# Kernel optimization log

Measured on AMD Instinct MI355X. Metric: run time of the kernel, lower is better.

The kernel has to match this reference:

```python
import jax, jax.numpy as jnp
import numpy as np

N = 100000   # nodes
E = 1600000  # edges
F = 128      # input features
H = 128      # hidden
O = 64       # output classes
BN_EPS = 1e-5


def gcn_conv(x, edge_index, W, b, n_nodes):
    """PyG-style GCNConv: h = D^-1/2 (A+I) D^-1/2 (x W) + b."""
    h = x @ W  # [N, out]
    row = jnp.concatenate([edge_index[0], jnp.arange(n_nodes)])  # add self loops
    col = jnp.concatenate([edge_index[1], jnp.arange(n_nodes)])
    deg = jax.ops.segment_sum(jnp.ones_like(row, dtype=h.dtype), row, num_segments=n_nodes)
    dinv = jnp.where(deg > 0, jax.lax.rsqrt(deg), 0.0)
    norm = dinv[row] * dinv[col]                 # [E+N]
    msg = h[col] * norm[:, None]                 # gather + scale
    out = jax.ops.segment_sum(msg, row, num_segments=n_nodes)  # scatter-add
    return out + b


def batch_norm(x, gamma, beta):
    mean = jnp.mean(x, axis=0)
    var = jnp.var(x, axis=0)
    return (x - mean) * jax.lax.rsqrt(var + BN_EPS) * gamma + beta


def setup_inputs() -> dict:
    key = jax.random.key(0)
    ks = jax.random.split(key, 10)
    x = jax.random.normal(ks[0], (N, F), dtype=jnp.float32)
    edge_index = jax.random.randint(ks[1], (2, E), 0, N, dtype=jnp.int64)
    W1 = jax.random.normal(ks[2], (F, H), dtype=jnp.float32) / np.sqrt(F)
    b1 = jnp.zeros((H,), dtype=jnp.float32)
    gamma1 = jnp.ones((H,), dtype=jnp.float32)
    beta1 = jnp.zeros((H,), dtype=jnp.float32)
    W2 = jax.random.normal(ks[3], (H, H), dtype=jnp.float32) / np.sqrt(H)
    b2 = jnp.zeros((H,), dtype=jnp.float32)
    W3 = jax.random.normal(ks[4], (H, O), dtype=jnp.float32) / np.sqrt(H)
    b3 = jnp.zeros((O,), dtype=jnp.float32)
    return {"x": x, "edge_index": edge_index, "W1": W1, "b1": b1,
            "gamma1": gamma1, "beta1": beta1, "W2": W2, "b2": b2,
            "W3": W3, "b3": b3}


def reference(x, edge_index, W1, b1, gamma1, beta1, W2, b2, W3, b3):
    h = gcn_conv(x, edge_index, W1, b1, N)
    h = jax.nn.relu(batch_norm(h, gamma1, beta1))
    h = gcn_conv(h, edge_index, W2, b2, N)
    h = jax.nn.relu(h)
    out = h @ W3 + b3  # final Linear classifier head [N, O]
    return out
```

## Files before the change

kernel.cpp:

```cpp
#include <hip/hip_runtime.h>

#define NN 100000
#define EE 1600000
#define HN 128
#define OO 64
#define SB 256
#define NBUCK 196
#define CH 4096

typedef __attribute__((ext_vector_type(8))) short bf16x8;
typedef __attribute__((ext_vector_type(4))) float f32x4;

__device__ __forceinline__ unsigned short f2bf(float f){
  unsigned u = __float_as_uint(f);
  return (unsigned short)((u + 0x7FFFu + ((u >> 16) & 1u)) >> 16);
}
__device__ __forceinline__ float bflo(unsigned u){ return __uint_as_float(u << 16); }
__device__ __forceinline__ float bfhi(unsigned u){ return __uint_as_float(u & 0xFFFF0000u); }

__global__ __launch_bounds__(256) void k_histpack(const int* __restrict__ rows, int* __restrict__ bcnt,
                                                  const float* __restrict__ W1, const float* __restrict__ W2,
                                                  const float* __restrict__ W3,
                                                  unsigned short* __restrict__ Wp1, unsigned short* __restrict__ Wp2,
                                                  unsigned short* __restrict__ Wp3){
  __shared__ int h[NBUCK];
  for (int i = threadIdx.x; i < NBUCK; i += 256) h[i] = 0;
  __syncthreads();
  int base = blockIdx.x * CH;
  for (int j = threadIdx.x; j < CH; j += 256){
    int e = base + j;
    if (e < EE) atomicAdd(&h[rows[e] >> 9], 1);
  }
  __syncthreads();
  for (int i = threadIdx.x; i < NBUCK; i += 256){
    int v = h[i];
    if (v) atomicAdd(&bcnt[i], v);
  }
  int b = blockIdx.x;
  if (b < 20){
    const float* W; unsigned short* Wp; int outc, i0;
    if (b < 8)      { W=W1; Wp=Wp1; outc=128; i0 = b*256; }
    else if (b < 16){ W=W2; Wp=Wp2; outc=128; i0 = (b-8)*256; }
    else            { W=W3; Wp=Wp3; outc=64;  i0 = (b-16)*256; }
    int i = i0 + threadIdx.x;
    if (i < 16*outc){
      int kb = i / outc, n = i - kb*outc;
      unsigned pk[4];
      #pragma unroll
      for (int jj = 0; jj < 4; ++jj){
        unsigned lo = f2bf(W[(size_t)(kb*8 + 2*jj)*outc + n]);
        unsigned hi = f2bf(W[(size_t)(kb*8 + 2*jj+1)*outc + n]);
        pk[jj] = lo | (hi << 16);
      }
      *reinterpret_cast<uint4*>(Wp + (size_t)i*8) = make_uint4(pk[0],pk[1],pk[2],pk[3]);
    }
  }
}

__global__ __launch_bounds__(64) void k_bscan(const int* __restrict__ bcnt,
                                              int* __restrict__ bbase, int* __restrict__ bcur){
  int lane = threadIdx.x;
  int run = 0;
  for (int c = 0; c < NBUCK; c += 64){
    int i = c + lane;
    int v = (i < NBUCK) ? bcnt[i] : 0;
    int s = v;
    #pragma unroll
    for (int d = 1; d < 64; d <<= 1){ int u = __shfl_up(s, d); if (lane >= d) s += u; }
    if (i < NBUCK){ bbase[i] = run + s - v; bcur[i] = run + s - v; }
    run += __shfl(s, 63);
  }
}

__global__ __launch_bounds__(256) void k_bucket(const int* __restrict__ rows, const int* __restrict__ cols,
                                                int* __restrict__ bcur, uint2* __restrict__ ebuf){
  __shared__ int bc[NBUCK];
  __shared__ int boff[NBUCK];
  __shared__ int ccur[NBUCK];
  __shared__ int gbase[NBUCK];
  __shared__ uint2 stage[CH];
  const int t = threadIdx.x;
  const int base = blockIdx.x * CH;
  const int nval = min(CH, EE - base);

  for (int i = t; i < NBUCK; i += 256) bc[i] = 0;
  __syncthreads();

  int er[16], ec[16];
  #pragma unroll
  for (int j = 0; j < 16; ++j){
    int i = j*256 + t;
    if (i < nval){
      er[j] = rows[base+i]; ec[j] = cols[base+i];
      atomicAdd(&bc[er[j] >> 9], 1);
    } else er[j] = -1;
  }
  __syncthreads();

  if (t < 64){
    int lane = t, run = 0;
    for (int c = 0; c < NBUCK; c += 64){
      int i = c + lane;
      int v = (i < NBUCK) ? bc[i] : 0;
      int s = v;
      #pragma unroll
      for (int d = 1; d < 64; d <<= 1){ int u = __shfl_up(s, d); if (lane >= d) s += u; }
      if (i < NBUCK) boff[i] = run + s - v;
      run += __shfl(s, 63);
    }
  }
  __syncthreads();
  if (t < NBUCK){
    gbase[t] = bc[t] ? atomicAdd(&bcur[t], bc[t]) : 0;
    ccur[t]  = boff[t];
  }
  __syncthreads();
  #pragma unroll
  for (int j = 0; j < 16; ++j){
    if (er[j] >= 0){
      int b = er[j] >> 9;
      int p = atomicAdd(&ccur[b], 1);
      stage[p] = make_uint2((unsigned)er[j], (unsigned)ec[j]);
    }
  }
  __syncthreads();
  for (int i = t; i < nval; i += 256){
    uint2 e = stage[i];
    int b = (int)(e.x >> 9);
    ebuf[gbase[b] + (i - boff[b])] = e;
  }
}

__global__ __launch_bounds__(256) void k_build(const uint2* __restrict__ ebuf,
                                               const int* __restrict__ bbase, const int* __restrict__ bcnt,
                                               int* __restrict__ row_start, int* __restrict__ cnt,
                                               float* __restrict__ dinv, int* __restrict__ csr_col){
  __shared__ int hist[512];
  __shared__ int cur[512];
  const int b = blockIdx.x;
  const int row0 = b << 9;
  const int nrow = min(512, NN - row0);
  const int ebase = bbase[b];
  const int ne = bcnt[b];
  const int t = threadIdx.x;

  for (int i = t; i < nrow; i += 256) hist[i] = 0;
  __syncthreads();
  for (int i = t; i < ne; i += 256)
    atomicAdd(&hist[(int)ebuf[ebase+i].x - row0], 1);
  __syncthreads();

  if (t < 64){
    int lane = t, run = 0;
    for (int c = 0; c < nrow; c += 64){
      int i = c + lane;
      int v = (i < nrow) ? hist[i] : 0;
      int s = v;
      #pragma unroll
      for (int d = 1; d < 64; d <<= 1){ int u = __shfl_up(s, d); if (lane >= d) s += u; }
      if (i < nrow) cur[i] = run + s - v;
      run += __shfl(s, 63);
    }
  }
  __syncthreads();
  for (int i = t; i < nrow; i += 256){
    int h = hist[i];
    int r = row0 + i;
    cnt[r] = h;
    dinv[r] = rsqrtf((float)(h+1));
    row_start[r] = ebase + cur[i];
    cur[i] += ebase;
  }
  __syncthreads();
  for (int i = t; i < ne; i += 256){
    uint2 e = ebuf[ebase+i];
    int p = atomicAdd(&cur[(int)e.x - row0], 1);
    csr_col[p] = (int)e.y;
  }
}

template<bool BF16OUT>
__global__ __launch_bounds__(256) void k_agg(const unsigned* __restrict__ h,
                                             const int* __restrict__ row_start,
                                             const int* __restrict__ cnt,
                                             const int* __restrict__ col,
                                             const float* __restrict__ dinv,
                                             const float* __restrict__ bias,
                                             void* __restrict__ outv){
  int wib  = __builtin_amdgcn_readfirstlane((int)(threadIdx.x >> 6));
  int wid  = blockIdx.x*4 + wib;
  int lane = threadIdx.x & 63;
  if (wid >= NN) return;
  int s = row_start[wid];
  int e = s + cnt[wid];
  float dr = dinv[wid];
  const unsigned* hp = h + lane;
  float ax, ay;
  {
    unsigned u = hp[(size_t)wid*64];
    ax = bflo(u); ay = bfhi(u);
  }
  int p = s;
  for (; p+7 < e; p += 8){
    unsigned uu[8];
    #pragma unroll
    for (int j=0;j<8;++j) uu[j] = hp[(size_t)col[p+j]*64];
    #pragma unroll
    for (int j=0;j<8;++j){ ax += bflo(uu[j]); ay += bfhi(uu[j]); }
  }
  for (; p+3 < e; p += 4){
    unsigned uu[4];
    #pragma unroll
    for (int j=0;j<4;++j) uu[j] = hp[(size_t)col[p+j]*64];
    #pragma unroll
    for (int j=0;j<4;++j){ ax += bflo(uu[j]); ay += bfhi(uu[j]); }
  }
  for (; p < e; ++p){
    unsigned u = hp[(size_t)col[p]*64];
    ax += bflo(u); ay += bfhi(u);
  }
  float2 bb = *reinterpret_cast<const float2*>(bias + 2*lane);
  float ox = ax*dr + bb.x, oy = ay*dr + bb.y;
  if constexpr (BF16OUT){
    ((unsigned*)outv)[(size_t)wid*64 + lane] = (unsigned)f2bf(ox) | ((unsigned)f2bf(oy) << 16);
  } else {
    *reinterpret_cast<float2*>((float*)outv + (size_t)wid*HN + 2*lane) = make_float2(ox, oy);
  }
}

template<int OUTC, int XFORM, bool ADD_BIAS, bool BF16OUT, bool ABF16>
__global__ __launch_bounds__(256) void k_mgemm(const void* __restrict__ Av,
                                               const unsigned short* __restrict__ Wp,
                                               const float* __restrict__ scale,
                                               const float* __restrict__ shiftv,
                                               const float* __restrict__ bias,
                                               const float* __restrict__ dinv,
                                               void* __restrict__ Cv){
  __shared__ char AsB[32768];
  const int t = threadIdx.x;
  const int row0 = blockIdx.x * 128;

  if constexpr (ABF16){
    const uint4* A = (const uint4*)Av;
    const int c8 = t & 15;
    const int k0 = c8*8;
    float sc[8], sh[8];
    if (XFORM == 1){
      #pragma unroll
      for (int j=0;j<8;++j){ sc[j]=scale[k0+j]; sh[j]=shiftv[k0+j]; }
    }
    #pragma unroll
    for (int g = 0; g < 8; ++g){
      int f = g*256 + t;
      int r = f >> 4;
      int row = row0 + r;
      int rc = row < NN ? row : NN-1;
      uint4 q = A[(size_t)rc*16 + c8];
      float vf[8] = { bflo(q.x),bfhi(q.x),bflo(q.y),bfhi(q.y),
                      bflo(q.z),bfhi(q.z),bflo(q.w),bfhi(q.w) };
      if (XFORM == 1){
        #pragma unroll
        for (int j=0;j<8;++j) vf[j] = fmaxf(fmaf(vf[j], sc[j], sh[j]), 0.f);
      } else if (XFORM == 2){
        #pragma unroll
        for (int j=0;j<8;++j) vf[j] = fmaxf(vf[j], 0.f);
      }
      unsigned pk[4];
      #pragma unroll
      for (int j=0;j<4;++j)
        pk[j] = (unsigned)f2bf(vf[2*j]) | ((unsigned)f2bf(vf[2*j+1]) << 16);
      int boff = (c8*16) ^ ((r & 7) << 4);
      *reinterpret_cast<uint4*>(AsB + r*256 + boff) = make_uint4(pk[0],pk[1],pk[2],pk[3]);
    }
  } else {
    const float* A = (const float*)Av;
    #pragma unroll
    for (int g = 0; g < 16; ++g){
      int f = g*256 + t;
      int r = f >> 5;
      int c4 = f & 31;
      int row = row0 + r;
      int rc = row < NN ? row : NN-1;
      float4 v = *reinterpret_cast<const float4*>(A + (size_t)rc*HN + c4*4);
      if (XFORM == 2){
        v.x = fmaxf(v.x, 0.f); v.y = fmaxf(v.y, 0.f);
        v.z = fmaxf(v.z, 0.f); v.w = fmaxf(v.w, 0.f);
      }
      unsigned p0 = (unsigned)f2bf(v.x) | ((unsigned)f2bf(v.y) << 16);
      unsigned p1 = (unsigned)f2bf(v.z) | ((unsigned)f2bf(v.w) << 16);
      int boff = (c4*8) ^ ((r & 7) << 4);
      *reinterpret_cast<uint2*>(AsB + r*256 + boff) = make_uint2(p0, p1);
    }
  }
  __syncthreads();

  const int wv = t >> 6;
  const int l  = t & 63;
  const int lm = l & 15;
  const int lk = l >> 4;
  constexpr int NF = OUTC/16;

  f32x4 acc[2][NF];
  #pragma unroll
  for (int mi=0;mi<2;++mi)
    #pragma unroll
    for (int ni=0;ni<NF;++ni) acc[mi][ni] = (f32x4){0.f,0.f,0.f,0.f};

  const bf16x8* WpV = reinterpret_cast<const bf16x8*>(Wp);

  #pragma unroll
  for (int ks = 0; ks < 4; ++ks){
    bf16x8 af[2];
    #pragma unroll
    for (int mi=0;mi<2;++mi){
      int R = wv*32 + mi*16 + lm;
      int boff = (ks*64 + lk*16) ^ ((R & 7) << 4);
      af[mi] = *reinterpret_cast<const bf16x8*>(AsB + R*256 + boff);
    }
    int kb = ks*4 + lk;
    #pragma unroll
    for (int ni=0;ni<NF;++ni){
      int n = ni*16 + lm;
      bf16x8 bfr = WpV[kb*OUTC + n];
      acc[0][ni] = __builtin_amdgcn_mfma_f32_16x16x32_bf16(af[0], bfr, acc[0][ni], 0,0,0);
      acc[1][ni] = __builtin_amdgcn_mfma_f32_16x16x32_bf16(af[1], bfr, acc[1][ni], 0,0,0);
    }
  }

  #pragma unroll
  for (int mi=0;mi<2;++mi){
    #pragma unroll
    for (int j=0;j<4;++j){
      int grow = row0 + wv*32 + mi*16 + lk*4 + j;
      if (grow >= NN) continue;
      if constexpr (BF16OUT){
        float dr = dinv[grow];
        unsigned short* po = (unsigned short*)Cv + (size_t)grow*OUTC;
        #pragma unroll
        for (int ni=0;ni<NF;++ni)
          po[ni*16 + lm] = f2bf(acc[mi][ni][j] * dr);
      } else {
        float* po = (float*)Cv + (size_t)grow*OUTC;
        #pragma unroll
        for (int ni=0;ni<NF;++ni){
          float v = acc[mi][ni][j];
          if (ADD_BIAS) v += bias[ni*16 + lm];
          po[ni*16 + lm] = v;
        }
      }
    }
  }
}

__global__ __launch_bounds__(256) void k_stats(const unsigned* __restrict__ a,
                                               float* __restrict__ ps, float* __restrict__ pq){
  __shared__ float l0[256], l1[256], m0[256], m1[256];
  int c = threadIdx.x & 63;
  int grp = threadIdx.x >> 6;
  float s0=0.f,s1=0.f,q0=0.f,q1=0.f;
  for (int r = blockIdx.x*4 + grp; r < NN; r += SB*4){
    unsigned u = a[(size_t)r*64 + c];
    float v0 = bflo(u), v1 = bfhi(u);
    s0 += v0; s1 += v1; q0 = fmaf(v0,v0,q0); q1 = fmaf(v1,v1,q1);
  }
  l0[threadIdx.x]=s0; l1[threadIdx.x]=s1; m0[threadIdx.x]=q0; m1[threadIdx.x]=q1;
  __syncthreads();
  if (grp==0){
    #pragma unroll
    for (int g=1;g<4;++g){ s0+=l0[g*64+c]; s1+=l1[g*64+c]; q0+=m0[g*64+c]; q1+=m1[g*64+c]; }
    ps[blockIdx.x*128 + 2*c]   = s0; ps[blockIdx.x*128 + 2*c+1] = s1;
    pq[blockIdx.x*128 + 2*c]   = q0; pq[blockIdx.x*128 + 2*c+1] = q1;
  }
}

__global__ __launch_bounds__(128) void k_bnfinal(const float* __restrict__ ps, const float* __restrict__ pq,
                                                 const float* __restrict__ gamma, const float* __restrict__ beta,
                                                 float* __restrict__ scale, float* __restrict__ shiftv){
  int c = threadIdx.x;
  float s=0.f, q=0.f;
  for (int b=0;b<SB;b++){ s += ps[b*128+c]; q += pq[b*128+c]; }
  float mean = s * (1.0f/NN);
  float var  = q * (1.0f/NN) - mean*mean;
  float inv  = rsqrtf(var + 1e-5f);
  float sc = gamma[c]*inv;
  scale[c]  = sc;
  shiftv[c] = beta[c] - mean*sc;
}

extern "C" void kernel_launch(void* const* d_in, const int* in_sizes, int n_in,
                              void* d_out, int out_size, void* d_ws, size_t ws_size,
                              hipStream_t stream) {
  const float* x      = (const float*)d_in[0];
  const int*   ei     = (const int*)d_in[1];
  const int*   rows   = ei;
  const int*   cols   = ei + EE;
  const float* W1     = (const float*)d_in[2];
  const float* b1     = (const float*)d_in[3];
  const float* gamma1 = (const float*)d_in[4];
  const float* beta1  = (const float*)d_in[5];
  const float* W2     = (const float*)d_in[6];
  const float* b2     = (const float*)d_in[7];
  const float* W3     = (const float*)d_in[8];
  const float* b3     = (const float*)d_in[9];
  float* out = (float*)d_out;

  char* w = (char*)d_ws;
  float* buf0      = (float*)w; w += (size_t)NN*HN*4;
  float* buf1      = (float*)w; w += (size_t)NN*HN*4;
  int*   csr_col   = (int*)w;   w += (size_t)EE*4;
  int*   row_start = (int*)w;   w += (size_t)NN*4;
  int*   cnt       = (int*)w;   w += (size_t)NN*4;
  float* dinv      = (float*)w; w += (size_t)NN*4;
  float* ps        = (float*)w; w += (size_t)SB*128*4;
  float* pq        = (float*)w; w += (size_t)SB*128*4;
  float* scale     = (float*)w; w += 1024;
  float* shiftv    = (float*)w; w += 1024;
  int*   bcnt      = (int*)w;   w += 1024;
  int*   bbase     = (int*)w;   w += 1024;
  int*   bcur      = (int*)w;   w += 1024;
  unsigned short* Wp1 = (unsigned short*)w; w += 128*128*2;
  unsigned short* Wp2 = (unsigned short*)w; w += 128*128*2;
  unsigned short* Wp3 = (unsigned short*)w; w += 128*64*2;
  uint2*    ebuf  = (uint2*)buf0;
  unsigned* hbf   = (unsigned*)buf0;
  unsigned* abf   = (unsigned*)buf1;

  (void)hipMemsetAsync(bcnt, 0, NBUCK*4, stream);

  const int CB = (EE + CH - 1)/CH, GB = (NN+127)/128, AB = NN/4;

  k_histpack<<<CB, 256, 0, stream>>>(rows, bcnt, W1, W2, W3, Wp1, Wp2, Wp3);
  k_bscan <<<1, 64, 0, stream>>>(bcnt, bbase, bcur);
  k_bucket<<<CB, 256, 0, stream>>>(rows, cols, bcur, ebuf);
  k_build <<<NBUCK, 256, 0, stream>>>(ebuf, bbase, bcnt, row_start, cnt, dinv, csr_col);

  k_mgemm<128,0,false,true,false><<<GB, 256, 0, stream>>>(x, Wp1, nullptr, nullptr, nullptr, dinv, hbf);
  k_agg<true><<<AB, 256, 0, stream>>>(hbf, row_start, cnt, csr_col, dinv, b1, abf);
  k_stats<<<SB, 256, 0, stream>>>(abf, ps, pq);
  k_bnfinal<<<1, 128, 0, stream>>>(ps, pq, gamma1, beta1, scale, shiftv);

  k_mgemm<128,1,false,true,true><<<GB, 256, 0, stream>>>(abf, Wp2, scale, shiftv, nullptr, dinv, hbf);
  k_agg<true><<<AB, 256, 0, stream>>>(hbf, row_start, cnt, csr_col, dinv, b2, abf);

  k_mgemm<64,2,true,false,true><<<GB, 256, 0, stream>>>(abf, Wp3, nullptr, nullptr, b3, nullptr, out);
}
```

Measured before the change: 274.1 us.

## Bucket edges into fixed-size slabs to drop histogram and scan passes

Edge bucketing now writes into fixed per-bucket slabs (SLAB entries each) using per-bucket atomic cursors. This removes the separate histogram kernel and the global bucket scan, and k_build computes its CSR base by summing the counts of earlier buckets. Each edge is also packed into a single 32-bit word (local row in the upper bits, column in the low 17 bits), which halves the staging traffic. The risk is overflow if any bucket receives more than SLAB edges, which is safe only for the roughly uniform random graph used here. Template parameters were also simplified.

```diff
diff --git a/kernel.cpp b/kernel.cpp
--- a/kernel.cpp
+++ b/kernel.cpp
@@ -7,6 +7,7 @@
 #define SB 256
 #define NBUCK 196
 #define CH 4096
+#define SLAB 16384
 
 typedef __attribute__((ext_vector_type(8))) short bf16x8;
 typedef __attribute__((ext_vector_type(4))) float f32x4;
@@ -18,31 +19,76 @@
 __device__ __forceinline__ float bflo(unsigned u){ return __uint_as_float(u << 16); }
 __device__ __forceinline__ float bfhi(unsigned u){ return __uint_as_float(u & 0xFFFF0000u); }
 
-__global__ __launch_bounds__(256) void k_histpack(const int* __restrict__ rows, int* __restrict__ bcnt,
-                                                  const float* __restrict__ W1, const float* __restrict__ W2,
-                                                  const float* __restrict__ W3,
-                                                  unsigned short* __restrict__ Wp1, unsigned short* __restrict__ Wp2,
-                                                  unsigned short* __restrict__ Wp3){
-  __shared__ int h[NBUCK];
-  for (int i = threadIdx.x; i < NBUCK; i += 256) h[i] = 0;
-  __syncthreads();
-  int base = blockIdx.x * CH;
-  for (int j = threadIdx.x; j < CH; j += 256){
-    int e = base + j;
-    if (e < EE) atomicAdd(&h[rows[e] >> 9], 1);
-  }
-  __syncthreads();
-  for (int i = threadIdx.x; i < NBUCK; i += 256){
-    int v = h[i];
-    if (v) atomicAdd(&bcnt[i], v);
-  }
+__global__ __launch_bounds__(256) void k_bucket(const int* __restrict__ rows, const int* __restrict__ cols,
+                                                int* __restrict__ pcur, unsigned* __restrict__ ebuf,
+                                                const float* __restrict__ W1, const float* __restrict__ W2,
+                                                const float* __restrict__ W3,
+                                                unsigned short* __restrict__ Wp1, unsigned short* __restrict__ Wp2,
+                                                unsigned short* __restrict__ Wp3){
+  __shared__ int bc[NBUCK];
+  __shared__ int boff[NBUCK];
+  __shared__ int ccur[NBUCK];
+  __shared__ int gbase[NBUCK];
+  __shared__ uint2 stage[CH];
+  const int t = threadIdx.x;
+  const int base = blockIdx.x * CH;
+  const int nval = min(CH, EE - base);
+
+  for (int i = t; i < NBUCK; i += 256) bc[i] = 0;
+  __syncthreads();
+
+  int er[16], ec[16];
+  #pragma unroll
+  for (int j = 0; j < 16; ++j){
+    int i = j*256 + t;
+    if (i < nval){
+      er[j] = rows[base+i]; ec[j] = cols[base+i];
+      atomicAdd(&bc[er[j] >> 9], 1);
+    } else er[j] = -1;
+  }
+  __syncthreads();
+
+  if (t < 64){
+    int lane = t, run = 0;
+    for (int c = 0; c < NBUCK; c += 64){
+      int i = c + lane;
+      int v = (i < NBUCK) ? bc[i] : 0;
+      int s = v;
+      #pragma unroll
+      for (int d = 1; d < 64; d <<= 1){ int u = __shfl_up(s, d); if (lane >= d) s += u; }
+      if (i < NBUCK) boff[i] = run + s - v;
+      run += __shfl(s, 63);
+    }
+  }
+  __syncthreads();
+  if (t < NBUCK){
+    gbase[t] = bc[t] ? (t*SLAB + atomicAdd(&pcur[t], bc[t])) : 0;
+    ccur[t]  = boff[t];
+  }
+  __syncthreads();
+  #pragma unroll
+  for (int j = 0; j < 16; ++j){
+    if (er[j] >= 0){
+      int b = er[j] >> 9;
+      int p = atomicAdd(&ccur[b], 1);
+      stage[p] = make_uint2((unsigned)er[j], (unsigned)ec[j]);
+    }
+  }
+  __syncthreads();
+  for (int i = t; i < nval; i += 256){
+    uint2 e = stage[i];
+    int b = (int)(e.x >> 9);
+    unsigned pk = ((e.x & 511u) << 17) | e.y;
+    ebuf[gbase[b] + (i - boff[b])] = pk;
+  }
+
   int b = blockIdx.x;
   if (b < 20){
     const float* W; unsigned short* Wp; int outc, i0;
     if (b < 8)      { W=W1; Wp=Wp1; outc=128; i0 = b*256; }
     else if (b < 16){ W=W2; Wp=Wp2; outc=128; i0 = (b-8)*256; }
     else            { W=W3; Wp=Wp3; outc=64;  i0 = (b-16)*256; }
-    int i = i0 + threadIdx.x;
+    int i = i0 + t;
     if (i < 16*outc){
       int kb = i / outc, n = i - kb*outc;
       unsigned pk[4];
@@ -57,97 +103,31 @@
   }
 }
 
-__global__ __launch_bounds__(64) void k_bscan(const int* __restrict__ bcnt,
-                                              int* __restrict__ bbase, int* __restrict__ bcur){
-  int lane = threadIdx.x;
-  int run = 0;
-  for (int c = 0; c < NBUCK; c += 64){
-    int i = c + lane;
-    int v = (i < NBUCK) ? bcnt[i] : 0;
-    int s = v;
-    #pragma unroll
-    for (int d = 1; d < 64; d <<= 1){ int u = __shfl_up(s, d); if (lane >= d) s += u; }
-    if (i < NBUCK){ bbase[i] = run + s - v; bcur[i] = run + s - v; }
-    run += __shfl(s, 63);
-  }
-}
-
-__global__ __launch_bounds__(256) void k_bucket(const int* __restrict__ rows, const int* __restrict__ cols,
-                                                int* __restrict__ bcur, uint2* __restrict__ ebuf){
-  __shared__ int bc[NBUCK];
-  __shared__ int boff[NBUCK];
-  __shared__ int ccur[NBUCK];
-  __shared__ int gbase[NBUCK];
-  __shared__ uint2 stage[CH];
-  const int t = threadIdx.x;
-  const int base = blockIdx.x * CH;
-  const int nval = min(CH, EE - base);
-
-  for (int i = t; i < NBUCK; i += 256) bc[i] = 0;
-  __syncthreads();
-
-  int er[16], ec[16];
-  #pragma unroll
-  for (int j = 0; j < 16; ++j){
-    int i = j*256 + t;
-    if (i < nval){
-      er[j] = rows[base+i]; ec[j] = cols[base+i];
-      atomicAdd(&bc[er[j] >> 9], 1);
-    } else er[j] = -1;
-  }
-  __syncthreads();
-
-  if (t < 64){
-    int lane = t, run = 0;
-    for (int c = 0; c < NBUCK; c += 64){
-      int i = c + lane;
-      int v = (i < NBUCK) ? bc[i] : 0;
-      int s = v;
-      #pragma unroll
-      for (int d = 1; d < 64; d <<= 1){ int u = __shfl_up(s, d); if (lane >= d) s += u; }
-      if (i < NBUCK) boff[i] = run + s - v;
-      run += __shfl(s, 63);
-    }
-  }
-  __syncthreads();
-  if (t < NBUCK){
-    gbase[t] = bc[t] ? atomicAdd(&bcur[t], bc[t]) : 0;
-    ccur[t]  = boff[t];
-  }
-  __syncthreads();
-  #pragma unroll
-  for (int j = 0; j < 16; ++j){
-    if (er[j] >= 0){
-      int b = er[j] >> 9;
-      int p = atomicAdd(&ccur[b], 1);
-      stage[p] = make_uint2((unsigned)er[j], (unsigned)ec[j]);
-    }
-  }
-  __syncthreads();
-  for (int i = t; i < nval; i += 256){
-    uint2 e = stage[i];
-    int b = (int)(e.x >> 9);
-    ebuf[gbase[b] + (i - boff[b])] = e;
-  }
-}
-
-__global__ __launch_bounds__(256) void k_build(const uint2* __restrict__ ebuf,
-                                               const int* __restrict__ bbase, const int* __restrict__ bcnt,
+__global__ __launch_bounds__(256) void k_build(const unsigned* __restrict__ ebuf,
+                                               const int* __restrict__ pcur,
                                                int* __restrict__ row_start, int* __restrict__ cnt,
                                                float* __restrict__ dinv, int* __restrict__ csr_col){
   __shared__ int hist[512];
   __shared__ int cur[512];
+  __shared__ int sCbase;
   const int b = blockIdx.x;
   const int row0 = b << 9;
   const int nrow = min(512, NN - row0);
-  const int ebase = bbase[b];
-  const int ne = bcnt[b];
+  const int ebase = b * SLAB;
+  const int ne = pcur[b];
   const int t = threadIdx.x;
 
+  if (t < 64){
+    int acc = 0;
+    for (int i = t; i < b; i += 64) acc += pcur[i];
+    #pragma unroll
+    for (int d = 32; d; d >>= 1) acc += __shfl_xor(acc, d);
+    if (t == 0) sCbase = acc;
+  }
   for (int i = t; i < nrow; i += 256) hist[i] = 0;
   __syncthreads();
   for (int i = t; i < ne; i += 256)
-    atomicAdd(&hist[(int)ebuf[ebase+i].x - row0], 1);
+    atomicAdd(&hist[ebuf[ebase+i] >> 17], 1);
   __syncthreads();
 
   if (t < 64){
@@ -163,30 +143,30 @@
     }
   }
   __syncthreads();
+  const int cbase = sCbase;
   for (int i = t; i < nrow; i += 256){
     int h = hist[i];
     int r = row0 + i;
     cnt[r] = h;
     dinv[r] = rsqrtf((float)(h+1));
-    row_start[r] = ebase + cur[i];
-    cur[i] += ebase;
+    row_start[r] = cbase + cur[i];
+    cur[i] += cbase;
   }
   __syncthreads();
   for (int i = t; i < ne; i += 256){
-    uint2 e = ebuf[ebase+i];
-    int p = atomicAdd(&cur[(int)e.x - row0], 1);
-    csr_col[p] = (int)e.y;
-  }
-}
-
-template<bool BF16OUT>
+    unsigned e = ebuf[ebase+i];
+    int p = atomicAdd(&cur[e >> 17], 1);
+    csr_col[p] = (int)(e & 0x1FFFFu);
+  }
+}
+
 __global__ __launch_bounds__(256) void k_agg(const unsigned* __restrict__ h,
                                              const int* __restrict__ row_start,
                                              const int* __restrict__ cnt,
                                              const int* __restrict__ col,
                                              const float* __restrict__ dinv,
                                              const float* __restrict__ bias,
-                                             void* __restrict__ outv){
+                                             unsigned* __restrict__ outv){
   int wib  = __builtin_amdgcn_readfirstlane((int)(threadIdx.x >> 6));
   int wid  = blockIdx.x*4 + wib;
   int lane = threadIdx.x & 63;
@@ -221,14 +201,10 @@
   }
   float2 bb = *reinterpret_cast<const float2*>(bias + 2*lane);
   float ox = ax*dr + bb.x, oy = ay*dr + bb.y;
-  if constexpr (BF16OUT){
-    ((unsigned*)outv)[(size_t)wid*64 + lane] = (unsigned)f2bf(ox) | ((unsigned)f2bf(oy) << 16);
-  } else {
-    *reinterpret_cast<float2*>((float*)outv + (size_t)wid*HN + 2*lane) = make_float2(ox, oy);
-  }
-}
-
-template<int OUTC, int XFORM, bool ADD_BIAS, bool BF16OUT, bool ABF16>
+  outv[(size_t)wid*64 + lane] = (unsigned)f2bf(ox) | ((unsigned)f2bf(oy) << 16);
+}
+
+template<int OUTC, int XFORM, bool BF16OUT, bool ABF16>
 __global__ __launch_bounds__(256) void k_mgemm(const void* __restrict__ Av,
                                                const unsigned short* __restrict__ Wp,
                                                const float* __restrict__ scale,
@@ -342,11 +318,8 @@
       } else {
         float* po = (float*)Cv + (size_t)grow*OUTC;
         #pragma unroll
-        for (int ni=0;ni<NF;++ni){
-          float v = acc[mi][ni][j];
-          if (ADD_BIAS) v += bias[ni*16 + lm];
-          po[ni*16 + lm] = v;
-        }
+        for (int ni=0;ni<NF;++ni)
+          po[ni*16 + lm] = acc[mi][ni][j] + bias[ni*16 + lm];
       }
     }
   }
@@ -415,32 +388,29 @@
   float* pq        = (float*)w; w += (size_t)SB*128*4;
   float* scale     = (float*)w; w += 1024;
   float* shiftv    = (float*)w; w += 1024;
-  int*   bcnt      = (int*)w;   w += 1024;
-  int*   bbase     = (int*)w;   w += 1024;
-  int*   bcur      = (int*)w;   w += 1024;
+  int*   scr0      = (int*)w;   w += 4096;
   unsigned short* Wp1 = (unsigned short*)w; w += 128*128*2;
   unsigned short* Wp2 = (unsigned short*)w; w += 128*128*2;
   unsigned short* Wp3 = (unsigned short*)w; w += 128*64*2;
-  uint2*    ebuf  = (uint2*)buf0;
-  unsigned* hbf   = (unsigned*)buf0;
-  unsigned* abf   = (unsigned*)buf1;
-
-  (void)hipMemsetAsync(bcnt, 0, NBUCK*4, stream);
+  int* pcur = scr0;
+  unsigned* ebuf = (unsigned*)buf0;
+  unsigned* hbf  = (unsigned*)buf0;
+  unsigned* abf  = (unsigned*)buf1;
+
+  (void)hipMemsetAsync(scr0, 0, 4096, stream);
 
   const int CB = (EE + CH - 1)/CH, GB = (NN+127)/128, AB = NN/4;
 
-  k_histpack<<<CB, 256, 0, stream>>>(rows, bcnt, W1, W2, W3, Wp1, Wp2, Wp3);
-  k_bscan <<<1, 64, 0, stream>>>(bcnt, bbase, bcur);
-  k_bucket<<<CB, 256, 0, stream>>>(rows, cols, bcur, ebuf);
-  k_build <<<NBUCK, 256, 0, stream>>>(ebuf, bbase, bcnt, row_start, cnt, dinv, csr_col);
-
-  k_mgemm<128,0,false,true,false><<<GB, 256, 0, stream>>>(x, Wp1, nullptr, nullptr, nullptr, dinv, hbf);
-  k_agg<true><<<AB, 256, 0, stream>>>(hbf, row_start, cnt, csr_col, dinv, b1, abf);
+  k_bucket<<<CB, 256, 0, stream>>>(rows, cols, pcur, ebuf, W1, W2, W3, Wp1, Wp2, Wp3);
+  k_build <<<NBUCK, 256, 0, stream>>>(ebuf, pcur, row_start, cnt, dinv, csr_col);
+
+  k_mgemm<128,0,true,false><<<GB, 256, 0, stream>>>(x, Wp1, nullptr, nullptr, nullptr, dinv, hbf);
+  k_agg<<<AB, 256, 0, stream>>>(hbf, row_start, cnt, csr_col, dinv, b1, abf);
   k_stats<<<SB, 256, 0, stream>>>(abf, ps, pq);
   k_bnfinal<<<1, 128, 0, stream>>>(ps, pq, gamma1, beta1, scale, shiftv);
 
-  k_mgemm<128,1,false,true,true><<<GB, 256, 0, stream>>>(abf, Wp2, scale, shiftv, nullptr, dinv, hbf);
-  k_agg<true><<<AB, 256, 0, stream>>>(hbf, row_start, cnt, csr_col, dinv, b2, abf);
-
-  k_mgemm<64,2,true,false,true><<<GB, 256, 0, stream>>>(abf, Wp3, nullptr, nullptr, b3, nullptr, out);
-}
+  k_mgemm<128,1,true,true><<<GB, 256, 0, stream>>>(abf, Wp2, scale, shiftv, nullptr, dinv, hbf);
+  k_agg<<<AB, 256, 0, stream>>>(hbf, row_start, cnt, csr_col, dinv, b2, abf);
+
+  k_mgemm<64,2,false,true><<<GB, 256, 0, stream>>>(abf, Wp3, nullptr, nullptr, b3, nullptr, out);
+}
```

Result: faster. 257.8 us (-5.9%).
